# Performance work log

Hardware: AMD Instinct MI355X
Metric: run time of the kernel (lower is better)

## Reference

```python
import jax, jax.numpy as jnp
import numpy as np

B = 64
N_IN = 1_000_000
N_OUT = 20_000
NNZ = 1_000_000
FILTERS = 1


def setup_inputs() -> dict:
    key = jax.random.key(0)
    k_x, k_w, k_o = jax.random.split(key, 3)
    x = jax.random.normal(k_x, (B, N_IN, 1), dtype=jnp.float32)
    # per-edge unshared weights (one per nonzero of the COO mask); scaled small
    kernel = jax.random.normal(k_w, (NNZ,), dtype=jnp.float32) * 0.05
    bias = jnp.zeros((N_OUT, FILTERS), dtype=jnp.float32)
    # COO mask: each input SNP connects to exactly one gene (sorted by output id)
    in_idx = jnp.arange(NNZ, dtype=jnp.int64)
    out_idx = jnp.sort(jax.random.randint(k_o, (NNZ,), 0, N_OUT, dtype=jnp.int64))
    return {"x": x, "kernel": kernel, "bias": bias,
            "in_idx": in_idx, "out_idx": out_idx, "n_out": N_OUT}


def reference(x, kernel, bias, in_idx, out_idx, n_out):
    # x: (B, steps, channels=1) -> flatten per-sample, as in local_conv_matmul_sparse
    b = x.shape[0]
    x_flat = x.reshape(b, -1)                       # (B, N_in)
    # sparse (N_out, N_in) @ x_flat.T expressed as gather * weight + segment_sum
    vals = x_flat[:, in_idx] * kernel[None, :]      # (B, nnz)
    out = jax.ops.segment_sum(vals.T, out_idx, num_segments=n_out)  # (N_out, B)
    out = out.T.reshape(b, n_out, 1)                # (B, N_out, filters=1)
    out = out + bias[None, :, :]                    # bias_add, channels_last
    return jnp.tanh(out)                            # activation='tanh'
```

## Files before the change

### kernel.cpp

```cpp
#include <hip/hip_runtime.h>
#include <cstdint>
#include <cstddef>


constexpr int EPW = 512;
constexpr int RPW = 16;
constexpr int WPB = 4;

#define DPP_SHR1 0x111
#define DPP_SHR2 0x112
#define DPP_SHR4 0x114
#define DPP_SHR8 0x118
#define DPP_BC15 0x142
#define DPP_BC31 0x143

#define SCAN_STEP(S, MF, CTRL, RM)                                                            \
    {                                                                                         \
        int _t = __builtin_amdgcn_update_dpp(0, __float_as_int(S), (CTRL), (RM), 0xF, true);  \
        (S) = fmaf((MF), __int_as_float(_t), (S));                                            \
    }

#define MAXS_STEP(R, CTRL, RM)                                                                \
    {                                                                                         \
        int _t = __builtin_amdgcn_update_dpp(0, (R), (CTRL), (RM), 0xF, true);                \
        (R) = max((R), _t);                                                                   \
    }

__device__ __forceinline__ void atomAddF(float* p, float v) {
    __hip_atomic_fetch_add(p, v, __ATOMIC_RELAXED, __HIP_MEMORY_SCOPE_AGENT);
}

__global__ __launch_bounds__(256)
void ld1d_zero(float* __restrict__ p, int n4, int ntot)
{
    int i = blockIdx.x * 256 + threadIdx.x;
    if (i < n4)
        *reinterpret_cast<float4*>(p + (size_t)i * 4) = make_float4(0.f, 0.f, 0.f, 0.f);
    if (blockIdx.x == 0 && threadIdx.x == 0)
        for (int k = n4 * 4; k < ntot; ++k) p[k] = 0.f;
}

__global__ __launch_bounds__(256)
void ld1d_accum(const float* __restrict__ x, const float* __restrict__ wgt,
                const int* __restrict__ in_idx, const int* __restrict__ out_idx,
                float* __restrict__ pre, int n_in, int nnz, int n_out, int batch, int wpw)
{
    const int lane = threadIdx.x & 63;
    const int gw   = blockIdx.x * WPB + (threadIdx.x >> 6);
    const int wid  = gw / wpw;
    const long long c0l = (long long)wid * EPW;
    if (c0l >= (long long)nnz) return;
    const int b0 = (gw - wid * wpw) * RPW;
    const int nrows = min(RPW, batch - b0);
    if (nrows <= 0) return;

    const int e0   = (int)c0l + lane * 8;
    const int last = nnz - 1;

    int   iv[8]; int ov[8]; float w[8];
    bool fok;
    if (e0 + 7 < nnz) {
        int4 i0 = *reinterpret_cast<const int4*>(in_idx + e0);
        int4 i1 = *reinterpret_cast<const int4*>(in_idx + e0 + 4);
        int4 o0 = *reinterpret_cast<const int4*>(out_idx + e0);
        int4 o1 = *reinterpret_cast<const int4*>(out_idx + e0 + 4);
        float4 w0 = *reinterpret_cast<const float4*>(wgt + e0);
        float4 w1 = *reinterpret_cast<const float4*>(wgt + e0 + 4);
        iv[0]=i0.x; iv[1]=i0.y; iv[2]=i0.z; iv[3]=i0.w; iv[4]=i1.x; iv[5]=i1.y; iv[6]=i1.z; iv[7]=i1.w;
        ov[0]=o0.x; ov[1]=o0.y; ov[2]=o0.z; ov[3]=o0.w; ov[4]=o1.x; ov[5]=o1.y; ov[6]=o1.z; ov[7]=o1.w;
        w[0]=w0.x; w[1]=w0.y; w[2]=w0.z; w[3]=w0.w; w[4]=w1.x; w[5]=w1.y; w[6]=w1.z; w[7]=w1.w;
        fok = true;
        #pragma unroll
        for (int k = 0; k < 8; ++k) fok = fok && (iv[k] == e0 + k);
    } else if (e0 < nnz) {
        #pragma unroll
        for (int k = 0; k < 8; ++k) {
            int a = min(e0 + k, last);
            iv[k] = in_idx[a]; ov[k] = out_idx[a];
            w[k]  = (e0 + k < nnz) ? wgt[a] : 0.f;
        }
        fok = false;
    } else {
        int o = out_idx[last];
        #pragma unroll
        for (int k = 0; k < 8; ++k) { iv[k] = 0; ov[k] = o; w[k] = 0.f; }
        fok = true;
    }
    const bool fast = (bool)__all((int)fok);

    bool bb[7]; float u[7];
    #pragma unroll
    for (int k = 0; k < 7; ++k) { bb[k] = (ov[k] != ov[k + 1]); u[k] = bb[k] ? 0.f : 1.f; }
    const bool hasB = bb[0] | bb[1] | bb[2] | bb[3] | bb[4] | bb[5] | bb[6];

    const int  pw   = __shfl_up(ov[7], 1);
    const bool cont = (lane > 0) && (ov[0] == pw);
    const bool fbrk = hasB || !cont;
    const int  fnext = __shfl_down((int)fbrk, 1);
    const bool Eend  = (lane == 63) || (fnext != 0);

    bool sfx[7];
    sfx[6] = bb[6];
    #pragma unroll
    for (int j = 5; j >= 1; --j) sfx[j] = bb[j] | sfx[j + 1];
    bool E[7];
    #pragma unroll
    for (int j = 1; j <= 6; ++j) E[j] = bb[j - 1] && sfx[j];
    const bool anyMid = (bool)__any((int)(E[1] | E[2] | E[3] | E[4] | E[5] | E[6]));

    int r = fbrk ? lane : 0;
    MAXS_STEP(r, DPP_SHR1, 0xF); MAXS_STEP(r, DPP_SHR2, 0xF);
    MAXS_STEP(r, DPP_SHR4, 0xF); MAXS_STEP(r, DPP_SHR8, 0xF);
    MAXS_STEP(r, DPP_BC15, 0xA); MAXS_STEP(r, DPP_BC31, 0xC);
    const float mf1  = (r <= lane - 1) ? 1.f : 0.f;
    const float mf2  = (r <= lane - 2) ? 1.f : 0.f;
    const float mf4  = (r <= lane - 4) ? 1.f : 0.f;
    const float mf8  = (r <= lane - 8) ? 1.f : 0.f;
    const float mf15 = (r <= (lane & ~15) - 1) ? 1.f : 0.f;
    const float mf31 = (r <= 31) ? 1.f : 0.f;

    const int nmax = n_in - 1;
    int ix[8];
    #pragma unroll
    for (int k = 0; k < 8; ++k) ix[k] = min(max(iv[k], 0), nmax);

    float* pb = pre + (size_t)b0 * (size_t)n_out;

    auto processRow = [&](const float q[8], float* pbr) {
        float t7 = q[7];
        float t6 = fmaf(u[6], t7, q[6]);
        float t5 = fmaf(u[5], t6, q[5]);
        float t4 = fmaf(u[4], t5, q[4]);
        float t3 = fmaf(u[3], t4, q[3]);
        float t2 = fmaf(u[2], t3, q[2]);
        float t1 = fmaf(u[1], t2, q[1]);
        float t0 = fmaf(u[0], t1, q[0]);
        float s = q[0];
        s = fmaf(u[0], s, q[1]); s = fmaf(u[1], s, q[2]); s = fmaf(u[2], s, q[3]);
        s = fmaf(u[3], s, q[4]); s = fmaf(u[4], s, q[5]); s = fmaf(u[5], s, q[6]);
        s = fmaf(u[6], s, q[7]);
        SCAN_STEP(s, mf1,  DPP_SHR1, 0xF);
        SCAN_STEP(s, mf2,  DPP_SHR2, 0xF);
        SCAN_STEP(s, mf4,  DPP_SHR4, 0xF);
        SCAN_STEP(s, mf8,  DPP_SHR8, 0xF);
        SCAN_STEP(s, mf15, DPP_BC15, 0xA);
        SCAN_STEP(s, mf31, DPP_BC31, 0xC);
        if (Eend) atomAddF(pbr + ov[7], s);
        if (hasB) atomAddF(pbr + ov[0], t0);
        if (anyMid) {
            if (E[1]) atomAddF(pbr + ov[1], t1);
            if (E[2]) atomAddF(pbr + ov[2], t2);
            if (E[3]) atomAddF(pbr + ov[3], t3);
            if (E[4]) atomAddF(pbr + ov[4], t4);
            if (E[5]) atomAddF(pbr + ov[5], t5);
            if (E[6]) atomAddF(pbr + ov[6], t6);
        }
    };

    if (fast) {
        const float*  xb = x + (size_t)b0 * (size_t)n_in + e0;
        const size_t  rs = (size_t)n_in;
        const int nb2 = nrows >> 1;
        float4 ca0, ca1, cb0, cb1;
        if (nb2 > 0) {
            ca0 = *reinterpret_cast<const float4*>(xb);
            ca1 = *reinterpret_cast<const float4*>(xb + 4);
            cb0 = *reinterpret_cast<const float4*>(xb + rs);
            cb1 = *reinterpret_cast<const float4*>(xb + rs + 4);
        }
        for (int ib = 0; ib < nb2; ++ib) {
            float4 na0, na1, nb0, nb1;
            const bool more = (2 * ib + 2) < (nb2 << 1);
            if (more) {
                const float* nx = xb + (size_t)(2 * ib + 2) * rs;
                na0 = *reinterpret_cast<const float4*>(nx);
                na1 = *reinterpret_cast<const float4*>(nx + 4);
                nb0 = *reinterpret_cast<const float4*>(nx + rs);
                nb1 = *reinterpret_cast<const float4*>(nx + rs + 4);
            }
            {
                float q[8] = { ca0.x * w[0], ca0.y * w[1], ca0.z * w[2], ca0.w * w[3],
                               ca1.x * w[4], ca1.y * w[5], ca1.z * w[6], ca1.w * w[7] };
                processRow(q, pb);
            }
            {
                float q[8] = { cb0.x * w[0], cb0.y * w[1], cb0.z * w[2], cb0.w * w[3],
                               cb1.x * w[4], cb1.y * w[5], cb1.z * w[6], cb1.w * w[7] };
                processRow(q, pb + n_out);
            }
            pb += 2 * (size_t)n_out;
            if (more) { ca0 = na0; ca1 = na1; cb0 = nb0; cb1 = nb1; }
        }
        if (nrows & 1) {
            const float* nx = xb + (size_t)(nrows - 1) * rs;
            float4 a0 = *reinterpret_cast<const float4*>(nx);
            float4 a1 = *reinterpret_cast<const float4*>(nx + 4);
            float q[8] = { a0.x * w[0], a0.y * w[1], a0.z * w[2], a0.w * w[3],
                           a1.x * w[4], a1.y * w[5], a1.z * w[6], a1.w * w[7] };
            processRow(q, pb);
        }
    } else {
        const float* xr = x + (size_t)b0 * (size_t)n_in;
        for (int i = 0; i < nrows; ++i) {
            float q[8];
            #pragma unroll
            for (int k = 0; k < 8; ++k) q[k] = xr[ix[k]] * w[k];
            processRow(q, pb);
            xr += (size_t)n_in; pb += (size_t)n_out;
        }
    }
}

__global__ __launch_bounds__(256)
void ld1d_finish_vec(float* __restrict__ out, const float* __restrict__ bias, int n_out4)
{
    const int o4 = blockIdx.x * 256 + threadIdx.x;
    if (o4 >= n_out4) return;
    const size_t flat = (size_t)blockIdx.y * (size_t)n_out4 * 4 + (size_t)o4 * 4;
    float4 v  = *reinterpret_cast<float4*>(out + flat);
    float4 bz = *reinterpret_cast<const float4*>(bias + (size_t)o4 * 4);
    v.x = tanhf(v.x + bz.x); v.y = tanhf(v.y + bz.y);
    v.z = tanhf(v.z + bz.z); v.w = tanhf(v.w + bz.w);
    *reinterpret_cast<float4*>(out + flat) = v;
}

__global__ __launch_bounds__(256)
void ld1d_finish_scalar(float* __restrict__ out, const float* __restrict__ bias,
                        int n_out, int ntot)
{
    int i = blockIdx.x * 256 + threadIdx.x;
    if (i >= ntot) return;
    int o = i % n_out;
    out[i] = tanhf(out[i] + bias[o]);
}

extern "C" void kernel_launch(void* const* d_in, const int* in_sizes, int n_in_arrs,
                              void* d_out, int out_size, void* d_ws, size_t ws_size,
                              hipStream_t stream)
{
    const float* x       = (const float*)d_in[0];
    const float* wgt     = (const float*)d_in[1];
    const float* bias    = (const float*)d_in[2];
    const int*   in_idx  = (const int*)d_in[3];
    const int*   out_idx = (const int*)d_in[4];
    float*       out     = (float*)d_out;

    const int nnz   = in_sizes[1];
    const int n_out = in_sizes[2];
    const int batch = out_size / n_out;
    const int n_in  = in_sizes[0] / batch;

    const int n4 = out_size / 4;
    hipLaunchKernelGGL(ld1d_zero, dim3((n4 + 255) / 256), dim3(256), 0, stream,
                       out, n4, out_size);

    const int nwin = (nnz + EPW - 1) / EPW;
    const int wpw  = (batch + RPW - 1) / RPW;
    const long long totalWaves = (long long)nwin * wpw;
    const int ablocks = (int)((totalWaves + WPB - 1) / WPB);
    hipLaunchKernelGGL(ld1d_accum, dim3(ablocks), dim3(256), 0, stream,
                       x, wgt, in_idx, out_idx, out, n_in, nnz, n_out, batch, wpw);

    if ((n_out & 3) == 0) {
        const int n_out4 = n_out / 4;
        hipLaunchKernelGGL(ld1d_finish_vec,
                           dim3((n_out4 + 255) / 256, batch), dim3(256), 0, stream,
                           out, bias, n_out4);
    } else {
        hipLaunchKernelGGL(ld1d_finish_scalar,
                           dim3((out_size + 255) / 256), dim3(256), 0, stream,
                           out, bias, n_out, out_size);
    }
}
```

Before: 60.53 us.

## Replace atomic scatter with output-partitioned fused segment reduction and tanh epilogue

Swaps the zero, atomic-accumulate and tanh-finish pipeline for two kernels. The first builds segment bounds (a CSR row pointer) from the sorted out_idx, and the second assigns each block a range of 16 output ids. Each wave streams that range's edges for 16 batch rows, carries partial sums across chunks in shared memory, and writes tanh(sum+bias) directly. This removes the atomics, the output zeroing pass and the separate finish pass, at the cost of an extra bounds kernel and only about 1250 blocks of 4 waves each. Segment boundaries that straddle chunks need careful carry handling.

```diff
diff --git a/kernel.cpp b/kernel.cpp
--- a/kernel.cpp
+++ b/kernel.cpp
@@ -3,9 +3,10 @@
 #include <cstddef>
 
 
+constexpr int OPB = 16;
+constexpr int WPB = 4;
+constexpr int RPW = 16;
 constexpr int EPW = 512;
-constexpr int RPW = 16;
-constexpr int WPB = 4;
 
 #define DPP_SHR1 0x111
 #define DPP_SHR2 0x112
@@ -26,212 +27,250 @@
         (R) = max((R), _t);                                                                   \
     }
 
-__device__ __forceinline__ void atomAddF(float* p, float v) {
-    __hip_atomic_fetch_add(p, v, __ATOMIC_RELAXED, __HIP_MEMORY_SCOPE_AGENT);
+__global__ __launch_bounds__(256)
+void ld1d_bounds(const int* __restrict__ out_idx, int* __restrict__ bnd,
+                 int nnz, int n_out)
+{
+    int e = blockIdx.x * 256 + threadIdx.x;
+    if (e >= nnz) return;
+    int cur  = out_idx[e];
+    int prev = (e == 0) ? -1 : out_idx[e - 1];
+    for (int o = prev + 1; o <= cur; ++o) bnd[o] = e;
+    if (e == nnz - 1)
+        for (int o = cur + 1; o <= n_out; ++o) bnd[o] = nnz;
 }
 
 __global__ __launch_bounds__(256)
-void ld1d_zero(float* __restrict__ p, int n4, int ntot)
+void ld1d_fused(const float* __restrict__ x, const float* __restrict__ wgt,
+                const float* __restrict__ bias, const int* __restrict__ in_idx,
+                const int* __restrict__ out_idx, const int* __restrict__ bnd,
+                float* __restrict__ out,
+                int n_in, int nnz, int n_out, int batch)
 {
-    int i = blockIdx.x * 256 + threadIdx.x;
-    if (i < n4)
-        *reinterpret_cast<float4*>(p + (size_t)i * 4) = make_float4(0.f, 0.f, 0.f, 0.f);
-    if (blockIdx.x == 0 && threadIdx.x == 0)
-        for (int k = n4 * 4; k < ntot; ++k) p[k] = 0.f;
-}
-
-__global__ __launch_bounds__(256)
-void ld1d_accum(const float* __restrict__ x, const float* __restrict__ wgt,
-                const int* __restrict__ in_idx, const int* __restrict__ out_idx,
-                float* __restrict__ pre, int n_in, int nnz, int n_out, int batch, int wpw)
-{
-    const int lane = threadIdx.x & 63;
-    const int gw   = blockIdx.x * WPB + (threadIdx.x >> 6);
-    const int wid  = gw / wpw;
-    const long long c0l = (long long)wid * EPW;
-    if (c0l >= (long long)nnz) return;
-    const int b0 = (gw - wid * wpw) * RPW;
+    __shared__ int   sbO[OPB + 1];
+    __shared__ float sbias[OPB];
+    __shared__ float cyl[WPB][RPW];
+
+    const int tid  = threadIdx.x;
+    const int lane = tid & 63;
+    const int wv   = tid >> 6;
+    const int O0   = blockIdx.x * OPB;
+    const int nO   = min(OPB, n_out - O0);
+
+    if (tid <= nO) sbO[tid] = bnd[min(O0 + tid, n_out)];
+    if (tid < nO)  sbias[tid] = bias[O0 + tid];
+    __syncthreads();
+
+    const int E0 = sbO[0];
+    const int E1 = sbO[nO];
+    const int b0 = wv * RPW;
     const int nrows = min(RPW, batch - b0);
-    if (nrows <= 0) return;
-
-    const int e0   = (int)c0l + lane * 8;
-    const int last = nnz - 1;
-
-    int   iv[8]; int ov[8]; float w[8];
-    bool fok;
-    if (e0 + 7 < nnz) {
-        int4 i0 = *reinterpret_cast<const int4*>(in_idx + e0);
-        int4 i1 = *reinterpret_cast<const int4*>(in_idx + e0 + 4);
-        int4 o0 = *reinterpret_cast<const int4*>(out_idx + e0);
-        int4 o1 = *reinterpret_cast<const int4*>(out_idx + e0 + 4);
-        float4 w0 = *reinterpret_cast<const float4*>(wgt + e0);
-        float4 w1 = *reinterpret_cast<const float4*>(wgt + e0 + 4);
-        iv[0]=i0.x; iv[1]=i0.y; iv[2]=i0.z; iv[3]=i0.w; iv[4]=i1.x; iv[5]=i1.y; iv[6]=i1.z; iv[7]=i1.w;
-        ov[0]=o0.x; ov[1]=o0.y; ov[2]=o0.z; ov[3]=o0.w; ov[4]=o1.x; ov[5]=o1.y; ov[6]=o1.z; ov[7]=o1.w;
-        w[0]=w0.x; w[1]=w0.y; w[2]=w0.z; w[3]=w0.w; w[4]=w1.x; w[5]=w1.y; w[6]=w1.z; w[7]=w1.w;
-        fok = true;
-        #pragma unroll
-        for (int k = 0; k < 8; ++k) fok = fok && (iv[k] == e0 + k);
-    } else if (e0 < nnz) {
-        #pragma unroll
-        for (int k = 0; k < 8; ++k) {
-            int a = min(e0 + k, last);
-            iv[k] = in_idx[a]; ov[k] = out_idx[a];
-            w[k]  = (e0 + k < nnz) ? wgt[a] : 0.f;
+
+    if (E1 > E0 && nrows > 0) {
+        if (lane < RPW) cyl[wv][lane] = 0.f;
+        const int olast = out_idx[E1 - 1];
+        const int CB = E0 & ~7;
+        int pend = -1;
+
+        for (int c0 = CB; c0 < E1; c0 += EPW) {
+            const int e0 = c0 + lane * 8;
+            const int nv = E1 - e0;
+
+            int iv[8]; int ov[8]; float w[8]; bool fok;
+            if (nv >= 8) {
+                int4 i0 = *reinterpret_cast<const int4*>(in_idx + e0);
+                int4 i1 = *reinterpret_cast<const int4*>(in_idx + e0 + 4);
+                int4 o0 = *reinterpret_cast<const int4*>(out_idx + e0);
+                int4 o1 = *reinterpret_cast<const int4*>(out_idx + e0 + 4);
+                float4 w0 = *reinterpret_cast<const float4*>(wgt + e0);
+                float4 w1 = *reinterpret_cast<const float4*>(wgt + e0 + 4);
+                iv[0]=i0.x; iv[1]=i0.y; iv[2]=i0.z; iv[3]=i0.w;
+                iv[4]=i1.x; iv[5]=i1.y; iv[6]=i1.z; iv[7]=i1.w;
+                ov[0]=o0.x; ov[1]=o0.y; ov[2]=o0.z; ov[3]=o0.w;
+                ov[4]=o1.x; ov[5]=o1.y; ov[6]=o1.z; ov[7]=o1.w;
+                w[0]=w0.x; w[1]=w0.y; w[2]=w0.z; w[3]=w0.w;
+                w[4]=w1.x; w[5]=w1.y; w[6]=w1.z; w[7]=w1.w;
+                fok = true;
+                #pragma unroll
+                for (int k = 0; k < 8; ++k) fok = fok && (iv[k] == e0 + k);
+            } else if (nv > 0) {
+                fok = true;
+                #pragma unroll
+                for (int k = 0; k < 8; ++k) {
+                    int a = min(e0 + k, E1 - 1);
+                    iv[k] = in_idx[a]; ov[k] = out_idx[a];
+                    if (k < nv) { w[k] = wgt[a]; fok = fok && (iv[k] == e0 + k); }
+                    else        { w[k] = 0.f; }
+                }
+            } else {
+                #pragma unroll
+                for (int k = 0; k < 8; ++k) { iv[k] = 0; ov[k] = olast; w[k] = 0.f; }
+                fok = true;
+            }
+            const bool fast = (bool)__all((int)fok);
+
+            bool bb[7]; float u[7];
+            #pragma unroll
+            for (int k = 0; k < 7; ++k) { bb[k] = (ov[k] != ov[k+1]); u[k] = bb[k] ? 0.f : 1.f; }
+            const bool hasB = bb[0]|bb[1]|bb[2]|bb[3]|bb[4]|bb[5]|bb[6];
+
+            const int  pw   = __shfl_up(ov[7], 1);
+            const bool cont = (lane > 0) && (ov[0] == pw);
+            const int  cnx  = __shfl_down((int)cont, 1);
+            const bool EendT = (lane < 63) && (cnx == 0);
+            const bool fbrk = hasB || !cont;
+
+            bool sfx[7];
+            sfx[6] = bb[6];
+            #pragma unroll
+            for (int j = 5; j >= 1; --j) sfx[j] = bb[j] | sfx[j+1];
+            bool E[7];
+            #pragma unroll
+            for (int j = 1; j <= 6; ++j) E[j] = bb[j-1] && sfx[j];
+
+            int r = fbrk ? lane : 0;
+            MAXS_STEP(r, DPP_SHR1, 0xF); MAXS_STEP(r, DPP_SHR2, 0xF);
+            MAXS_STEP(r, DPP_SHR4, 0xF); MAXS_STEP(r, DPP_SHR8, 0xF);
+            MAXS_STEP(r, DPP_BC15, 0xA); MAXS_STEP(r, DPP_BC31, 0xC);
+            const float mf1  = (r <= lane - 1) ? 1.f : 0.f;
+            const float mf2  = (r <= lane - 2) ? 1.f : 0.f;
+            const float mf4  = (r <= lane - 4) ? 1.f : 0.f;
+            const float mf8  = (r <= lane - 8) ? 1.f : 0.f;
+            const float mf15 = (r <= (lane & ~15) - 1) ? 1.f : 0.f;
+            const float mf31 = (r <= 31) ? 1.f : 0.f;
+
+            const int firsto = __builtin_amdgcn_readlane(ov[0], 0);
+            const int lasto  = __builtin_amdgcn_readlane(ov[7], 63);
+            const bool single = (firsto == lasto);
+
+            if (pend >= 0 && pend != firsto) {
+                if ((unsigned)(pend - O0) < (unsigned)nO && lane < nrows)
+                    out[(size_t)(b0 + lane) * n_out + pend] =
+                        tanhf(cyl[wv][lane] + sbias[pend - O0]);
+                if (lane < RPW) cyl[wv][lane] = 0.f;
+            }
+            pend = lasto;
+
+            const int nmax = n_in - 1;
+            int ix[8];
+            #pragma unroll
+            for (int k = 0; k < 8; ++k) ix[k] = min(max(iv[k], 0), nmax);
+
+            const bool ldv = fast && (nv > 0) && (e0 + 8 <= n_in);
+            const bool lds_ = fast && (nv > 0) && !(e0 + 8 <= n_in);
+
+            float* pbr = out + (size_t)b0 * (size_t)n_out;
+
+            auto processRow = [&](const float4& a0, const float4& a1, int i, float* pr) {
+                float q0, q1, q2, q3, q4, q5, q6, q7;
+                q0 = a0.x * w[0]; q1 = a0.y * w[1]; q2 = a0.z * w[2]; q3 = a0.w * w[3];
+                q4 = a1.x * w[4]; q5 = a1.y * w[5]; q6 = a1.z * w[6]; q7 = a1.w * w[7];
+                const float cy = cyl[wv][i];
+                float t6 = fmaf(u[6], q7, q6);
+                float t5 = fmaf(u[5], t6, q5);
+                float t4 = fmaf(u[4], t5, q4);
+                float t3 = fmaf(u[3], t4, q3);
+                float t2 = fmaf(u[2], t3, q2);
+                float t1 = fmaf(u[1], t2, q1);
+                float t0 = fmaf(u[0], t1, q0);
+                float s = q0;
+                s = fmaf(u[0], s, q1); s = fmaf(u[1], s, q2); s = fmaf(u[2], s, q3);
+                s = fmaf(u[3], s, q4); s = fmaf(u[4], s, q5); s = fmaf(u[5], s, q6);
+                s = fmaf(u[6], s, q7);
+                SCAN_STEP(s, mf1,  DPP_SHR1, 0xF);
+                SCAN_STEP(s, mf2,  DPP_SHR2, 0xF);
+                SCAN_STEP(s, mf4,  DPP_SHR4, 0xF);
+                SCAN_STEP(s, mf8,  DPP_SHR8, 0xF);
+                SCAN_STEP(s, mf15, DPP_BC15, 0xA);
+                SCAN_STEP(s, mf31, DPP_BC31, 0xC);
+                const float sp = __shfl_up(s, 1);
+                if (EendT) {
+                    const int o = ov[7];
+                    if ((unsigned)(o - O0) < (unsigned)nO) {
+                        float v = s + ((o == firsto) ? cy : 0.f);
+                        pr[o] = tanhf(v + sbias[o - O0]);
+                    }
+                }
+                if (hasB) {
+                    const int o = ov[0];
+                    if ((unsigned)(o - O0) < (unsigned)nO) {
+                        float v = t0;
+                        if (cont) v += sp;
+                        if (o == firsto) v += cy;
+                        pr[o] = tanhf(v + sbias[o - O0]);
+                    }
+                }
+                if (E[1] && (unsigned)(ov[1]-O0) < (unsigned)nO) pr[ov[1]] = tanhf(t1 + sbias[ov[1]-O0]);
+                if (E[2] && (unsigned)(ov[2]-O0) < (unsigned)nO) pr[ov[2]] = tanhf(t2 + sbias[ov[2]-O0]);
+                if (E[3] && (unsigned)(ov[3]-O0) < (unsigned)nO) pr[ov[3]] = tanhf(t3 + sbias[ov[3]-O0]);
+                if (E[4] && (unsigned)(ov[4]-O0) < (unsigned)nO) pr[ov[4]] = tanhf(t4 + sbias[ov[4]-O0]);
+                if (E[5] && (unsigned)(ov[5]-O0) < (unsigned)nO) pr[ov[5]] = tanhf(t5 + sbias[ov[5]-O0]);
+                if (E[6] && (unsigned)(ov[6]-O0) < (unsigned)nO) pr[ov[6]] = tanhf(t6 + sbias[ov[6]-O0]);
+                float cyn = __int_as_float(__builtin_amdgcn_readlane(__float_as_int(s), 63));
+                if (single) cyn += cy;
+                if (lane == 0) cyl[wv][i] = cyn;
+            };
+
+            const float4 Z4 = make_float4(0.f, 0.f, 0.f, 0.f);
+            auto loadRow = [&](int i, float4& a0, float4& a1) {
+                if (ldv) {
+                    const float* p = x + (size_t)(b0 + i) * (size_t)n_in + e0;
+                    a0 = *reinterpret_cast<const float4*>(p);
+                    a1 = *reinterpret_cast<const float4*>(p + 4);
+                } else if (lds_) {
+                    const float* p = x + (size_t)(b0 + i) * (size_t)n_in;
+                    a0 = make_float4(p[ix[0]], p[ix[1]], p[ix[2]], p[ix[3]]);
+                    a1 = make_float4(p[ix[4]], p[ix[5]], p[ix[6]], p[ix[7]]);
+                } else {
+                    a0 = Z4; a1 = Z4;
+                }
+            };
+
+            if (fast) {
+                const int nb2 = nrows >> 1;
+                float4 ca0, ca1, cb0, cb1;
+                if (nb2 > 0) { loadRow(0, ca0, ca1); loadRow(1, cb0, cb1); }
+                for (int ib = 0; ib < nb2; ++ib) {
+                    float4 na0, na1, nb0_, nb1_;
+                    const bool more = (2*ib + 2) < nrows;
+                    if (more) {
+                        loadRow(2*ib + 2, na0, na1);
+                        if (2*ib + 3 < nrows) loadRow(2*ib + 3, nb0_, nb1_);
+                        else { nb0_ = Z4; nb1_ = Z4; }
+                    }
+                    processRow(ca0, ca1, 2*ib,     pbr + (size_t)(2*ib) * n_out);
+                    processRow(cb0, cb1, 2*ib + 1, pbr + (size_t)(2*ib + 1) * n_out);
+                    if (more) { ca0 = na0; ca1 = na1; cb0 = nb0_; cb1 = nb1_; }
+                }
+                if (nrows & 1) {
+                    float4 a0, a1;
+                    loadRow(nrows - 1, a0, a1);
+                    processRow(a0, a1, nrows - 1, pbr + (size_t)(nrows - 1) * n_out);
+                }
+            } else {
+                for (int i = 0; i < nrows; ++i) {
+                    const float* p = x + (size_t)(b0 + i) * (size_t)n_in;
+                    float4 a0 = make_float4(p[ix[0]], p[ix[1]], p[ix[2]], p[ix[3]]);
+                    float4 a1 = make_float4(p[ix[4]], p[ix[5]], p[ix[6]], p[ix[7]]);
+                    if (nv <= 0) { a0 = Z4; a1 = Z4; }
+                    processRow(a0, a1, i, pbr + (size_t)i * n_out);
+                }
+            }
         }
-        fok = false;
-    } else {
-        int o = out_idx[last];
-        #pragma unroll
-        for (int k = 0; k < 8; ++k) { iv[k] = 0; ov[k] = o; w[k] = 0.f; }
-        fok = true;
+
+        if (pend >= 0 && (unsigned)(pend - O0) < (unsigned)nO && lane < nrows)
+            out[(size_t)(b0 + lane) * n_out + pend] =
+                tanhf(cyl[wv][lane] + sbias[pend - O0]);
     }
-    const bool fast = (bool)__all((int)fok);
-
-    bool bb[7]; float u[7];
-    #pragma unroll
-    for (int k = 0; k < 7; ++k) { bb[k] = (ov[k] != ov[k + 1]); u[k] = bb[k] ? 0.f : 1.f; }
-    const bool hasB = bb[0] | bb[1] | bb[2] | bb[3] | bb[4] | bb[5] | bb[6];
-
-    const int  pw   = __shfl_up(ov[7], 1);
-    const bool cont = (lane > 0) && (ov[0] == pw);
-    const bool fbrk = hasB || !cont;
-    const int  fnext = __shfl_down((int)fbrk, 1);
-    const bool Eend  = (lane == 63) || (fnext != 0);
-
-    bool sfx[7];
-    sfx[6] = bb[6];
-    #pragma unroll
-    for (int j = 5; j >= 1; --j) sfx[j] = bb[j] | sfx[j + 1];
-    bool E[7];
-    #pragma unroll
-    for (int j = 1; j <= 6; ++j) E[j] = bb[j - 1] && sfx[j];
-    const bool anyMid = (bool)__any((int)(E[1] | E[2] | E[3] | E[4] | E[5] | E[6]));
-
-    int r = fbrk ? lane : 0;
-    MAXS_STEP(r, DPP_SHR1, 0xF); MAXS_STEP(r, DPP_SHR2, 0xF);
-    MAXS_STEP(r, DPP_SHR4, 0xF); MAXS_STEP(r, DPP_SHR8, 0xF);
-    MAXS_STEP(r, DPP_BC15, 0xA); MAXS_STEP(r, DPP_BC31, 0xC);
-    const float mf1  = (r <= lane - 1) ? 1.f : 0.f;
-    const float mf2  = (r <= lane - 2) ? 1.f : 0.f;
-    const float mf4  = (r <= lane - 4) ? 1.f : 0.f;
-    const float mf8  = (r <= lane - 8) ? 1.f : 0.f;
-    const float mf15 = (r <= (lane & ~15) - 1) ? 1.f : 0.f;
-    const float mf31 = (r <= 31) ? 1.f : 0.f;
-
-    const int nmax = n_in - 1;
-    int ix[8];
-    #pragma unroll
-    for (int k = 0; k < 8; ++k) ix[k] = min(max(iv[k], 0), nmax);
-
-    float* pb = pre + (size_t)b0 * (size_t)n_out;
-
-    auto processRow = [&](const float q[8], float* pbr) {
-        float t7 = q[7];
-        float t6 = fmaf(u[6], t7, q[6]);
-        float t5 = fmaf(u[5], t6, q[5]);
-        float t4 = fmaf(u[4], t5, q[4]);
-        float t3 = fmaf(u[3], t4, q[3]);
-        float t2 = fmaf(u[2], t3, q[2]);
-        float t1 = fmaf(u[1], t2, q[1]);
-        float t0 = fmaf(u[0], t1, q[0]);
-        float s = q[0];
-        s = fmaf(u[0], s, q[1]); s = fmaf(u[1], s, q[2]); s = fmaf(u[2], s, q[3]);
-        s = fmaf(u[3], s, q[4]); s = fmaf(u[4], s, q[5]); s = fmaf(u[5], s, q[6]);
-        s = fmaf(u[6], s, q[7]);
-        SCAN_STEP(s, mf1,  DPP_SHR1, 0xF);
-        SCAN_STEP(s, mf2,  DPP_SHR2, 0xF);
-        SCAN_STEP(s, mf4,  DPP_SHR4, 0xF);
-        SCAN_STEP(s, mf8,  DPP_SHR8, 0xF);
-        SCAN_STEP(s, mf15, DPP_BC15, 0xA);
-        SCAN_STEP(s, mf31, DPP_BC31, 0xC);
-        if (Eend) atomAddF(pbr + ov[7], s);
-        if (hasB) atomAddF(pbr + ov[0], t0);
-        if (anyMid) {
-            if (E[1]) atomAddF(pbr + ov[1], t1);
-            if (E[2]) atomAddF(pbr + ov[2], t2);
-            if (E[3]) atomAddF(pbr + ov[3], t3);
-            if (E[4]) atomAddF(pbr + ov[4], t4);
-            if (E[5]) atomAddF(pbr + ov[5], t5);
-            if (E[6]) atomAddF(pbr + ov[6], t6);
-        }
-    };
-
-    if (fast) {
-        const float*  xb = x + (size_t)b0 * (size_t)n_in + e0;
-        const size_t  rs = (size_t)n_in;
-        const int nb2 = nrows >> 1;
-        float4 ca0, ca1, cb0, cb1;
-        if (nb2 > 0) {
-            ca0 = *reinterpret_cast<const float4*>(xb);
-            ca1 = *reinterpret_cast<const float4*>(xb + 4);
-            cb0 = *reinterpret_cast<const float4*>(xb + rs);
-            cb1 = *reinterpret_cast<const float4*>(xb + rs + 4);
-        }
-        for (int ib = 0; ib < nb2; ++ib) {
-            float4 na0, na1, nb0, nb1;
-            const bool more = (2 * ib + 2) < (nb2 << 1);
-            if (more) {
-                const float* nx = xb + (size_t)(2 * ib + 2) * rs;
-                na0 = *reinterpret_cast<const float4*>(nx);
-                na1 = *reinterpret_cast<const float4*>(nx + 4);
-                nb0 = *reinterpret_cast<const float4*>(nx + rs);
-                nb1 = *reinterpret_cast<const float4*>(nx + rs + 4);
+
+    if (nrows > 0) {
+        for (int k = 0; k < nO; ++k) {
+            if (sbO[k] == sbO[k + 1]) {
+                if (lane < nrows)
+                    out[(size_t)(b0 + lane) * n_out + (O0 + k)] = tanhf(sbias[k]);
             }
-            {
-                float q[8] = { ca0.x * w[0], ca0.y * w[1], ca0.z * w[2], ca0.w * w[3],
-                               ca1.x * w[4], ca1.y * w[5], ca1.z * w[6], ca1.w * w[7] };
-                processRow(q, pb);
-            }
-            {
-                float q[8] = { cb0.x * w[0], cb0.y * w[1], cb0.z * w[2], cb0.w * w[3],
-                               cb1.x * w[4], cb1.y * w[5], cb1.z * w[6], cb1.w * w[7] };
-                processRow(q, pb + n_out);
-            }
-            pb += 2 * (size_t)n_out;
-            if (more) { ca0 = na0; ca1 = na1; cb0 = nb0; cb1 = nb1; }
-        }
-        if (nrows & 1) {
-            const float* nx = xb + (size_t)(nrows - 1) * rs;
-            float4 a0 = *reinterpret_cast<const float4*>(nx);
-            float4 a1 = *reinterpret_cast<const float4*>(nx + 4);
-            float q[8] = { a0.x * w[0], a0.y * w[1], a0.z * w[2], a0.w * w[3],
-                           a1.x * w[4], a1.y * w[5], a1.z * w[6], a1.w * w[7] };
-            processRow(q, pb);
-        }
-    } else {
-        const float* xr = x + (size_t)b0 * (size_t)n_in;
-        for (int i = 0; i < nrows; ++i) {
-            float q[8];
-            #pragma unroll
-            for (int k = 0; k < 8; ++k) q[k] = xr[ix[k]] * w[k];
-            processRow(q, pb);
-            xr += (size_t)n_in; pb += (size_t)n_out;
         }
     }
-}
-
-__global__ __launch_bounds__(256)
-void ld1d_finish_vec(float* __restrict__ out, const float* __restrict__ bias, int n_out4)
-{
-    const int o4 = blockIdx.x * 256 + threadIdx.x;
-    if (o4 >= n_out4) return;
-    const size_t flat = (size_t)blockIdx.y * (size_t)n_out4 * 4 + (size_t)o4 * 4;
-    float4 v  = *reinterpret_cast<float4*>(out + flat);
-    float4 bz = *reinterpret_cast<const float4*>(bias + (size_t)o4 * 4);
-    v.x = tanhf(v.x + bz.x); v.y = tanhf(v.y + bz.y);
-    v.z = tanhf(v.z + bz.z); v.w = tanhf(v.w + bz.w);
-    *reinterpret_cast<float4*>(out + flat) = v;
-}
-
-__global__ __launch_bounds__(256)
-void ld1d_finish_scalar(float* __restrict__ out, const float* __restrict__ bias,
-                        int n_out, int ntot)
-{
-    int i = blockIdx.x * 256 + threadIdx.x;
-    if (i >= ntot) return;
-    int o = i % n_out;
-    out[i] = tanhf(out[i] + bias[o]);
 }
 
 extern "C" void kernel_launch(void* const* d_in, const int* in_sizes, int n_in_arrs,
@@ -244,31 +283,18 @@
     const int*   in_idx  = (const int*)d_in[3];
     const int*   out_idx = (const int*)d_in[4];
     float*       out     = (float*)d_out;
+    int*         bnd     = (int*)d_ws;
 
     const int nnz   = in_sizes[1];
     const int n_out = in_sizes[2];
     const int batch = out_size / n_out;
     const int n_in  = in_sizes[0] / batch;
 
-    const int n4 = out_size / 4;
-    hipLaunchKernelGGL(ld1d_zero, dim3((n4 + 255) / 256), dim3(256), 0, stream,
-                       out, n4, out_size);
-
-    const int nwin = (nnz + EPW - 1) / EPW;
-    const int wpw  = (batch + RPW - 1) / RPW;
-    const long long totalWaves = (long long)nwin * wpw;
-    const int ablocks = (int)((totalWaves + WPB - 1) / WPB);
-    hipLaunchKernelGGL(ld1d_accum, dim3(ablocks), dim3(256), 0, stream,
-                       x, wgt, in_idx, out_idx, out, n_in, nnz, n_out, batch, wpw);
-
-    if ((n_out & 3) == 0) {
-        const int n_out4 = n_out / 4;
-        hipLaunchKernelGGL(ld1d_finish_vec,
-                           dim3((n_out4 + 255) / 256, batch), dim3(256), 0, stream,
-                           out, bias, n_out4);
-    } else {
-        hipLaunchKernelGGL(ld1d_finish_scalar,
-                           dim3((out_size + 255) / 256), dim3(256), 0, stream,
-                           out, bias, n_out, out_size);
-    }
+    hipLaunchKernelGGL(ld1d_bounds, dim3((nnz + 255) / 256), dim3(256), 0, stream,
+                       out_idx, bnd, nnz, n_out);
+
+    const int blocks = (n_out + OPB - 1) / OPB;
+    hipLaunchKernelGGL(ld1d_fused, dim3(blocks), dim3(256), 0, stream,
+                       x, wgt, bias, in_idx, out_idx, bnd, out,
+                       n_in, nnz, n_out, batch);
 }
```

Result: slower. 95.68 us (+58.1%).
